# Optimization experiments

Hardware: AMD Instinct MI355X
Metric: run time of the kernel (lower is better)

The kernel has to match this reference:

```python
import jax, jax.numpy as jnp
import numpy as np

N, E, D, A = 50000, 1_600_000, 32, 2
H1, C1, H2, C2 = 4, 16, 2, 32  # GATv2Conv(D,16,heads=4) -> 64; GATv2Conv(64,32,heads=2) -> 64


def setup_inputs() -> dict:
    key = jax.random.key(0)
    ks = jax.random.split(key, 16)

    def glorot(k, shape):
        fan = shape[0] + shape[-1]
        return jax.random.normal(k, shape, jnp.float32) * np.float32(np.sqrt(2.0 / fan))

    return {
        "x": jax.random.normal(ks[0], (N, D), jnp.float32),
        "edge_index": jax.random.randint(ks[1], (2, E), 0, N),
        "edge_attr": jax.random.normal(ks[2], (E, 2), jnp.float32),
        # GATv2 layer 1 (lin_l/lin_r with bias, lin_edge no bias, att [H,C], out bias)
        "w1_l": glorot(ks[3], (D, H1 * C1)), "b1_l": jnp.zeros((H1 * C1,), jnp.float32),
        "w1_r": glorot(ks[4], (D, H1 * C1)), "b1_r": jnp.zeros((H1 * C1,), jnp.float32),
        "w1_e": glorot(ks[5], (2, H1 * C1)),
        "att1": glorot(ks[6], (H1, C1)),
        "bias1": jnp.zeros((H1 * C1,), jnp.float32),
        # GATv2 layer 2
        "w2_l": glorot(ks[7], (H1 * C1, H2 * C2)), "b2_l": jnp.zeros((H2 * C2,), jnp.float32),
        "w2_r": glorot(ks[8], (H1 * C1, H2 * C2)), "b2_r": jnp.zeros((H2 * C2,), jnp.float32),
        "w2_e": glorot(ks[9], (2, H2 * C2)),
        "att2": glorot(ks[10], (H2, C2)),
        "bias2": jnp.zeros((H2 * C2,), jnp.float32),
        # heads
        "w_actor": glorot(ks[11], (H2 * C2, A)), "b_actor": jnp.zeros((A,), jnp.float32),
        "w_critic": glorot(ks[12], (H2 * C2, 1)), "b_critic": jnp.zeros((1,), jnp.float32),
        "log_std": jnp.zeros((A,), jnp.float32),
    }


def _gatv2(x, src, dst, eattr, Wl, bl, Wr, br, We, att, bias, H, C, n):
    # PyG GATv2Conv: message j->i with i = dst, j = src
    xl = (x @ Wl + bl).reshape(n, H, C)  # source-side transform (x_j)
    xr = (x @ Wr + br).reshape(n, H, C)  # target-side transform (x_i)
    ee = (eattr @ We).reshape(-1, H, C)  # per-edge embedding
    z = jax.nn.leaky_relu(xl[src] + xr[dst] + ee, 0.2)  # [Etot, H, C]
    logits = jnp.einsum('ehc,hc->eh', z, att)  # [Etot, H]
    # segment softmax over incoming edges of each dst node
    m = jax.ops.segment_max(logits, dst, num_segments=n)
    p = jnp.exp(logits - m[dst])
    denom = jax.ops.segment_sum(p, dst, num_segments=n)
    alpha = p / denom[dst]  # every node has a self-loop -> denom > 0
    msg = xl[src] * alpha[:, :, None]  # [Etot, H, C]
    out = jax.ops.segment_sum(msg, dst, num_segments=n)
    return out.reshape(n, H * C) + bias


def reference(x, edge_index, edge_attr,
              w1_l, b1_l, w1_r, b1_r, w1_e, att1, bias1,
              w2_l, b2_l, w2_r, b2_r, w2_e, att2, bias2,
              w_actor, b_actor, w_critic, b_critic, log_std):
    src, dst = edge_index[0], edge_index[1]
    # add_self_loops=True, fill_value='mean': self-loop edge_attr = mean of incoming edge_attr
    cnt = jax.ops.segment_sum(jnp.ones((edge_attr.shape[0],), x.dtype), dst, num_segments=N)
    sums = jax.ops.segment_sum(edge_attr, dst, num_segments=N)
    loop_attr = sums / jnp.maximum(cnt, 1.0)[:, None]
    loop = jnp.arange(N, dtype=src.dtype)
    src_f = jnp.concatenate([src, loop])
    dst_f = jnp.concatenate([dst, loop])
    ea = jnp.concatenate([edge_attr, loop_attr], axis=0)

    h = jax.nn.relu(_gatv2(x, src_f, dst_f, ea, w1_l, b1_l, w1_r, b1_r, w1_e, att1, bias1, H1, C1, N))
    h = jax.nn.relu(_gatv2(h, src_f, dst_f, ea, w2_l, b2_l, w2_r, b2_r, w2_e, att2, bias2, H2, C2, N))

    action_mean = jnp.tanh(h @ w_actor + b_actor)  # [N, A]
    value = h @ w_critic + b_critic               # [N, 1]
    std = jnp.exp(log_std)                        # [A]  (Normal(action_mean, std))
    return action_mean, std, value
```

## Files before the change

kernel.cpp:

```cpp
#include <hip/hip_runtime.h>
#include <hip/hip_fp16.h>
#include <math.h>

#define DIN   32
#define F1    64
#define F2    64

typedef __attribute__((ext_vector_type(2))) float f32x2;

__device__ __forceinline__ f32x2 pkfma(f32x2 a, f32x2 b, f32x2 c) {
#if __has_builtin(__builtin_elementwise_fma)
    return __builtin_elementwise_fma(a, b, c);
#else
    return a * b + c;
#endif
}
__device__ __forceinline__ f32x2 pkmax(f32x2 a, f32x2 b) {
    f32x2 r; r.x = fmaxf(a.x, b.x); r.y = fmaxf(a.y, b.y); return r;
}

__device__ __forceinline__ unsigned bf16pack(float a, float b) {
    unsigned ua = __float_as_uint(a);
    unsigned ub = __float_as_uint(b);
    ua = (ua + 0x7FFFu + ((ua >> 16) & 1u)) >> 16;
    ub = (ub + 0x7FFFu + ((ub >> 16) & 1u)) >> 16;
    return ua | (ub << 16);
}

template <int K>
__device__ __forceinline__ void lin_lr_body(int bid,
        const float* __restrict__ x,
        const float* __restrict__ Wl, const float* __restrict__ bl,
        const float* __restrict__ Wr, const float* __restrict__ br,
        __half* __restrict__ xl, float* __restrict__ xr, int n) {
    __shared__ float Ash[32][K + 4];
    __shared__ float Wsh[K][128];
    const int t = threadIdx.x;
    const int node0 = bid * 32;

    for (int idx = t; idx < 32 * (K / 4); idx += 256) {
        int m = idx / (K / 4), kq = idx % (K / 4);
        float4 v = make_float4(0.f, 0.f, 0.f, 0.f);
        if (node0 + m < n) v = ((const float4*)(x + (size_t)(node0 + m) * K))[kq];
        *(float4*)&Ash[m][kq * 4] = v;
    }
    for (int idx = t; idx < K * 32; idx += 256) {
        int k = idx / 32, j4 = idx % 32;
        float4 v = (j4 < 16) ? ((const float4*)(Wl + (size_t)k * 64))[j4]
                             : ((const float4*)(Wr + (size_t)k * 64))[j4 - 16];
        *(float4*)&Wsh[k][j4 * 4] = v;
    }
    __syncthreads();

    const int ty = t >> 4;
    const int tx = t & 15;
    f32x2 c0[4], c1[4];
#pragma unroll
    for (int j = 0; j < 4; j++) {
        c0[j].x = 0.f; c0[j].y = 0.f;
        c1[j].x = 0.f; c1[j].y = 0.f;
    }

#pragma unroll 4
    for (int k = 0; k < K; k++) {
        float a0 = Ash[ty * 2 + 0][k];
        float a1 = Ash[ty * 2 + 1][k];
        float4 w0 = *(const float4*)&Wsh[k][tx * 8];
        float4 w1 = *(const float4*)&Wsh[k][tx * 8 + 4];
        f32x2 wv0; wv0.x = w0.x; wv0.y = w0.y;
        f32x2 wv1; wv1.x = w0.z; wv1.y = w0.w;
        f32x2 wv2; wv2.x = w1.x; wv2.y = w1.y;
        f32x2 wv3; wv3.x = w1.z; wv3.y = w1.w;
        f32x2 a0s; a0s.x = a0; a0s.y = a0;
        f32x2 a1s; a1s.x = a1; a1s.y = a1;
        c0[0] = pkfma(a0s, wv0, c0[0]);
        c0[1] = pkfma(a0s, wv1, c0[1]);
        c0[2] = pkfma(a0s, wv2, c0[2]);
        c0[3] = pkfma(a0s, wv3, c0[3]);
        c1[0] = pkfma(a1s, wv0, c1[0]);
        c1[1] = pkfma(a1s, wv1, c1[1]);
        c1[2] = pkfma(a1s, wv2, c1[2]);
        c1[3] = pkfma(a1s, wv3, c1[3]);
    }

    const float* bsrc = (tx < 8) ? bl : br;
    int jb = (tx < 8) ? tx * 8 : (tx - 8) * 8;
    float4 b0 = ((const float4*)(bsrc + jb))[0];
    float4 b1 = ((const float4*)(bsrc + jb))[1];
#pragma unroll
    for (int m = 0; m < 2; m++) {
        int node = node0 + ty * 2 + m;
        if (node >= n) continue;
        const f32x2* cc = (m == 0) ? c0 : c1;
        float o0 = cc[0].x + b0.x, o1 = cc[0].y + b0.y;
        float o2 = cc[1].x + b0.z, o3 = cc[1].y + b0.w;
        float o4 = cc[2].x + b1.x, o5 = cc[2].y + b1.y;
        float o6 = cc[3].x + b1.z, o7 = cc[3].y + b1.w;
        if (tx < 8) {
            __half2 h0 = __floats2half2_rn(o0, o1);
            __half2 h1 = __floats2half2_rn(o2, o3);
            __half2 h2 = __floats2half2_rn(o4, o5);
            __half2 h3 = __floats2half2_rn(o6, o7);
            uint4 pk;
            pk.x = *(unsigned*)&h0; pk.y = *(unsigned*)&h1;
            pk.z = *(unsigned*)&h2; pk.w = *(unsigned*)&h3;
            *((uint4*)(xl + (size_t)node * 64 + jb)) = pk;
        } else {
            float4 f0 = make_float4(o0, o1, o2, o3);
            float4 f1 = make_float4(o4, o5, o6, o7);
            ((float4*)(xr + (size_t)node * 64 + jb))[0] = f0;
            ((float4*)(xr + (size_t)node * 64 + jb))[1] = f1;
        }
    }
}

__global__ __launch_bounds__(512, 2)
void count_scatter(const int* __restrict__ srcr, const int* __restrict__ dstr,
                   const float* __restrict__ ea, int* __restrict__ cursor,
                   int2* __restrict__ inter, int E, int Ec, int NB, int cap) {
    __shared__ int2 recsh[3584];
    __shared__ unsigned short rksh[3584];
    __shared__ unsigned char bksh[3584];
    __shared__ int hist[256];
    __shared__ int colsh[256];
    const int blk = blockIdx.x;
    const int t = threadIdx.x;
    if (t < 256) hist[t] = 0;
    __syncthreads();
    const int s0 = blk * Ec, s1 = min(E, s0 + Ec);
    const int cnt = s1 - s0;
    for (int e = s0 + t; e < s1; e += 512) {
        int d = dstr[e];
        float2 v = ((const float2*)ea)[e];
        int2 r;
        r.x = srcr[e] | ((d & 255) << 24);
        r.y = (int)bf16pack(v.x, v.y);
        int li = e - s0;
        int bk = (unsigned)d >> 8;
        recsh[li] = r;
        bksh[li] = (unsigned char)bk;
        rksh[li] = (unsigned short)atomicAdd(&hist[bk], 1);
    }
    __syncthreads();
    if (t < NB) {
        int h = hist[t];
        colsh[t] = t * cap + (h ? atomicAdd(&cursor[t], h) : 0);
    }
    __syncthreads();
    for (int li = t; li < cnt; li += 512)
        inter[colsh[bksh[li]] + (int)rksh[li]] = recsh[li];
}

__global__ __launch_bounds__(256, 2)
void fused_csr_lin1(const int2* __restrict__ inter, const int* __restrict__ cursor,
                    int2* __restrict__ rse, int2* __restrict__ edges,
                    int NB, int N, int cap,
                    const float* __restrict__ x,
                    const float* __restrict__ Wl, const float* __restrict__ bl,
                    const float* __restrict__ Wr, const float* __restrict__ br,
                    __half* __restrict__ xl, float* __restrict__ xr, int n) {
    if ((int)blockIdx.x >= NB) {
        lin_lr_body<DIN>(blockIdx.x - NB, x, Wl, bl, Wr, br, xl, xr, n);
        return;
    }
    __shared__ int sh[256];
    __shared__ int cur[256];
    const int b = blockIdx.x, t = threadIdx.x;
    const int bstart = b * cap;
    const int bend = bstart + cursor[b];

    sh[t] = 0;
    __syncthreads();
    for (int pos = bstart + t; pos < bend; pos += 256)
        atomicAdd(&sh[((unsigned)inter[pos].x) >> 24], 1);
    __syncthreads();
    int cnt_v = sh[t];
    __syncthreads();
    sh[t] = cnt_v;
    __syncthreads();
    for (int off = 1; off < 256; off <<= 1) {
        int xv = (t >= off) ? sh[t - off] : 0;
        __syncthreads();
        sh[t] += xv;
        __syncthreads();
    }
    {
        int excl = sh[t] - cnt_v;
        cur[t] = excl;
        int myrs = bstart + excl;
        int node = b * 256 + t;
        if (node < N) rse[node] = make_int2(myrs, myrs + cnt_v);
    }
    __syncthreads();
    for (int pos = bstart + t; pos < bend; pos += 256) {
        int2 r = inter[pos];
        int k = atomicAdd(&cur[((unsigned)r.x) >> 24], 1);
        r.x &= 0x00FFFFFF;
        edges[bstart + k] = r;
    }
    int zend = (b + 1) * cap + ((b == NB - 1) ? 64 : 0);
    for (int pos = bend + t; pos < zend; pos += 256)
        edges[pos] = make_int2(0, 0);
}

template <int H, int C, bool FUSE_HEADS, bool FUSE_LIN2>
__global__ __launch_bounds__(512)
void gat_kernel(const __half* __restrict__ xl, const float* __restrict__ xr,
                const int2* __restrict__ rse,
                const int2* __restrict__ edges,
                const float* __restrict__ We, const float* __restrict__ att,
                const float* __restrict__ bias, float* __restrict__ hout,
                const float* __restrict__ w2l, const float* __restrict__ b2l,
                const float* __restrict__ w2r, const float* __restrict__ b2r,
                __half* __restrict__ xl2o, float* __restrict__ xr2o,
                const float* __restrict__ wa, const float* __restrict__ ba,
                const float* __restrict__ wc, const float* __restrict__ bc,
                const float* __restrict__ ls, float* __restrict__ pout,
                int n) {
    constexpr int LPH = C / 4;
    __shared__ float W2sh[FUSE_LIN2 ? 64 * 128 : 4];
    if constexpr (FUSE_LIN2) {
        for (int idx = threadIdx.x; idx < 64 * 32; idx += (int)blockDim.x) {
            int k = idx >> 5, j4 = idx & 31;
            float4 v = (j4 < 16) ? ((const float4*)(w2l + (size_t)k * 64))[j4]
                                 : ((const float4*)(w2r + (size_t)k * 64))[j4 - 16];
            *(float4*)&W2sh[k * 128 + j4 * 4] = v;
        }
        __syncthreads();
    }
    if (FUSE_HEADS && blockIdx.x == 0 && threadIdx.x < 2)
        pout[(size_t)n * 2 + threadIdx.x] = expf(ls[threadIdx.x]);
    const int lane = threadIdx.x & 63;
    const int wid = (blockIdx.x * blockDim.x + threadIdx.x) >> 6;
    if (wid >= n) return;
    const int i = wid;
    const int g = lane >> 4;
    const int q = lane & 15;

    const uint2* xlh = (const uint2*)xl;
    const float4 xri4 = ((const float4*)(xr + (size_t)i * 64))[q];
    const float4 we04 = ((const float4*)We)[q];
    const float4 we14 = ((const float4*)(We + 64))[q];
    const float4 av4 = ((const float4*)att)[q];
    const float LOG2E = 1.4426950408889634f;
    f32x2 xrlo; xrlo.x = xri4.x; xrlo.y = xri4.y;
    f32x2 xrhi; xrhi.x = xri4.z; xrhi.y = xri4.w;
    f32x2 we0lo; we0lo.x = we04.x; we0lo.y = we04.y;
    f32x2 we0hi; we0hi.x = we04.z; we0hi.y = we04.w;
    f32x2 we1lo; we1lo.x = we14.x; we1lo.y = we14.y;
    f32x2 we1hi; we1hi.x = we14.z; we1hi.y = we14.w;
    f32x2 avlo; avlo.x = av4.x * LOG2E; avlo.y = av4.y * LOG2E;
    f32x2 avhi; avhi.x = av4.z * LOG2E; avhi.y = av4.w * LOG2E;

    auto h4lo = [](uint2 h) -> f32x2 {
        float2 a = __half22float2(*(__half2*)&h.x);
        f32x2 r; r.x = a.x; r.y = a.y; return r;
    };
    auto h4hi = [](uint2 h) -> f32x2 {
        float2 b = __half22float2(*(__half2*)&h.y);
        f32x2 r; r.x = b.x; r.y = b.y; return r;
    };
    auto logit_of = [&](f32x2 xlo, f32x2 xhi, float ea0, float ea1) -> float {
        f32x2 e0; e0.x = ea0; e0.y = ea0;
        f32x2 e1; e1.x = ea1; e1.y = ea1;
        f32x2 ylo = xlo + pkfma(e0, we0lo, pkfma(e1, we1lo, xrlo));
        f32x2 yhi = xhi + pkfma(e0, we0hi, pkfma(e1, we1hi, xrhi));
        ylo = pkmax(ylo, ylo * 0.2f);
        yhi = pkmax(yhi, yhi * 0.2f);
        f32x2 l2 = pkfma(ylo, avlo, yhi * avhi);
        return l2.x + l2.y;
    };

    float den = 0.f;
    float sea0 = 0.f, sea1 = 0.f;
    f32x2 aclo; aclo.x = 0.f; aclo.y = 0.f;
    f32x2 achi; achi.x = 0.f; achi.y = 0.f;

    const int2 se = rse[i];
    const int e0 = se.x, e1 = se.y;
    const int r = (e1 - e0) & 7;

    if (r) {
        int2 h0 = edges[e0 + g];
        int2 h1 = edges[e0 + 4 + g];
        uint2 u0 = xlh[(h0.x << 4) + q];
        uint2 u1 = xlh[(h1.x << 4) + q];
        f32x2 x0lo = h4lo(u0), x0hi = h4hi(u0);
        f32x2 x1lo = h4lo(u1), x1hi = h4hi(u1);
        const bool v0 = g < r;
        const bool v1 = (4 + g) < r;
        float ea00 = v0 ? __int_as_float(h0.y << 16) : 0.f;
        float ea01 = v0 ? __int_as_float(h0.y & 0xFFFF0000) : 0.f;
        float ea10 = v1 ? __int_as_float(h1.y << 16) : 0.f;
        float ea11 = v1 ? __int_as_float(h1.y & 0xFFFF0000) : 0.f;
        sea0 += ea00 + ea10;
        sea1 += ea01 + ea11;
        float l0 = logit_of(x0lo, x0hi, ea00, ea01);
        float l1 = logit_of(x1lo, x1hi, ea10, ea11);
#pragma unroll
        for (int m = 1; m < LPH; m <<= 1) {
            l0 += __shfl_xor(l0, m, 64);
            l1 += __shfl_xor(l1, m, 64);
        }
        float p0 = v0 ? exp2f(l0) : 0.f;
        float p1 = v1 ? exp2f(l1) : 0.f;
        den += p0 + p1;
        f32x2 p0s; p0s.x = p0; p0s.y = p0;
        f32x2 p1s; p1s.x = p1; p1s.y = p1;
        aclo = pkfma(p0s, x0lo, pkfma(p1s, x1lo, aclo));
        achi = pkfma(p0s, x0hi, pkfma(p1s, x1hi, achi));
    }

    const int em = e0 + r;
    int2 rn0 = edges[em + g];
    int2 rn1 = edges[em + 4 + g];
    uint2 xpn0 = xlh[(rn0.x << 4) + q];
    uint2 xpn1 = xlh[(rn1.x << 4) + q];

    for (int eb = em; eb < e1; eb += 8) {
        int2 r0 = rn0, r1 = rn1;
        f32x2 x0lo = h4lo(xpn0), x0hi = h4hi(xpn0);
        f32x2 x1lo = h4lo(xpn1), x1hi = h4hi(xpn1);
        rn0 = edges[eb + 8 + g];
        rn1 = edges[eb + 12 + g];
        xpn0 = xlh[(rn0.x << 4) + q];
        xpn1 = xlh[(rn1.x << 4) + q];

        float ea00 = __int_as_float(r0.y << 16);
        float ea01 = __int_as_float(r0.y & 0xFFFF0000);
        float ea10 = __int_as_float(r1.y << 16);
        float ea11 = __int_as_float(r1.y & 0xFFFF0000);
        sea0 += ea00 + ea10;
        sea1 += ea01 + ea11;

        float l0 = logit_of(x0lo, x0hi, ea00, ea01);
        float l1 = logit_of(x1lo, x1hi, ea10, ea11);
#pragma unroll
        for (int m = 1; m < LPH; m <<= 1) {
            l0 += __shfl_xor(l0, m, 64);
            l1 += __shfl_xor(l1, m, 64);
        }
        float p0 = exp2f(l0);
        float p1 = exp2f(l1);
        den += p0 + p1;
        f32x2 p0s; p0s.x = p0; p0s.y = p0;
        f32x2 p1s; p1s.x = p1; p1s.y = p1;
        aclo = pkfma(p0s, x0lo, pkfma(p1s, x1lo, aclo));
        achi = pkfma(p0s, x0hi, pkfma(p1s, x1hi, achi));
    }

    float a0 = aclo.x, a1 = aclo.y, a2 = achi.x, a3 = achi.y;

#pragma unroll
    for (int m = 16; m < 64; m <<= 1) {
        den += __shfl_xor(den, m, 64);
        a0 += __shfl_xor(a0, m, 64);
        a1 += __shfl_xor(a1, m, 64);
        a2 += __shfl_xor(a2, m, 64);
        a3 += __shfl_xor(a3, m, 64);
        sea0 += __shfl_xor(sea0, m, 64);
        sea1 += __shfl_xor(sea1, m, 64);
    }

    const int cnt_i = e1 - e0;
    const float invc = cnt_i ? 1.0f / (float)cnt_i : 0.f;
    const float lamx = sea0 * invc;
    const float lamy = sea1 * invc;
    uint2 us = xlh[(i << 4) + q];
    f32x2 xslo = h4lo(us), xshi = h4hi(us);
    {
        float l = logit_of(xslo, xshi, lamx, lamy);
#pragma unroll
        for (int m = 1; m < LPH; m <<= 1) l += __shfl_xor(l, m, 64);
        float p = exp2f(l);
        den += p;
        a0 = fmaf(p, xslo.x, a0);
        a1 = fmaf(p, xslo.y, a1);
        a2 = fmaf(p, xshi.x, a2);
        a3 = fmaf(p, xshi.y, a3);
    }

    float rd = 1.0f / den;
    const float4 bv = ((const float4*)bias)[q];
    float4 o;
    o.x = fmaxf(fmaf(a0, rd, bv.x), 0.f);
    o.y = fmaxf(fmaf(a1, rd, bv.y), 0.f);
    o.z = fmaxf(fmaf(a2, rd, bv.z), 0.f);
    o.w = fmaxf(fmaf(a3, rd, bv.w), 0.f);

    if constexpr (FUSE_LIN2) {
        const int hl = lane & 31;
        const bool isl = lane < 32;
        f32x2 s; s.x = 0.f; s.y = 0.f;
#pragma unroll
        for (int k = 0; k < 64; k++) {
            float comp = ((k & 3) == 0) ? o.x : ((k & 3) == 1) ? o.y
                       : ((k & 3) == 2) ? o.z : o.w;
            float hk = __uint_as_float(
                __builtin_amdgcn_readlane(__float_as_uint(comp), k >> 2));
            f32x2 hs; hs.x = hk; hs.y = hk;
            f32x2 wv = *(const f32x2*)&W2sh[k * 128 + 2 * lane];
            s = pkfma(hs, wv, s);
        }
        const float* bsel = isl ? b2l : b2r;
        s.x += bsel[2 * hl];
        s.y += bsel[2 * hl + 1];
        if (isl) {
            __half2 hx = __floats2half2_rn(s.x, s.y);
            *(unsigned*)(xl2o + (size_t)i * 64 + 2 * hl) = *(unsigned*)&hx;
        } else {
            ((float2*)(xr2o + (size_t)i * 64))[hl] = make_float2(s.x, s.y);
        }
    } else if (!FUSE_HEADS) {
        if (g == 0) ((float4*)(hout + (size_t)i * 64))[q] = o;
    } else {
        float4 wa01 = ((const float4*)wa)[q * 2];
        float4 wa23 = ((const float4*)wa)[q * 2 + 1];
        float4 wcv  = ((const float4*)wc)[q];
        float d0 = o.x * wa01.x + o.y * wa01.z + o.z * wa23.x + o.w * wa23.z;
        float d1 = o.x * wa01.y + o.y * wa01.w + o.z * wa23.y + o.w * wa23.w;
        float d2 = o.x * wcv.x + o.y * wcv.y + o.z * wcv.z + o.w * wcv.w;
#pragma unroll
        for (int m = 1; m < 16; m <<= 1) {
            d0 += __shfl_xor(d0, m, 64);
            d1 += __shfl_xor(d1, m, 64);
            d2 += __shfl_xor(d2, m, 64);
        }
        if (lane == 0) {
            pout[(size_t)i * 2 + 0] = tanhf(d0 + ba[0]);
            pout[(size_t)i * 2 + 1] = tanhf(d1 + ba[1]);
            pout[(size_t)n * 2 + 2 + i] = d2 + bc[0];
        }
    }
}


extern "C" void kernel_launch(void* const* d_in, const int* in_sizes, int n_in,
                              void* d_out, int out_size, void* d_ws, size_t ws_size,
                              hipStream_t stream) {
    const float* x    = (const float*)d_in[0];
    const int*   ei   = (const int*)  d_in[1];
    const float* ea   = (const float*)d_in[2];
    const float* w1l  = (const float*)d_in[3];
    const float* b1l  = (const float*)d_in[4];
    const float* w1r  = (const float*)d_in[5];
    const float* b1r  = (const float*)d_in[6];
    const float* w1e  = (const float*)d_in[7];
    const float* att1 = (const float*)d_in[8];
    const float* bias1= (const float*)d_in[9];
    const float* w2l  = (const float*)d_in[10];
    const float* b2l  = (const float*)d_in[11];
    const float* w2r  = (const float*)d_in[12];
    const float* b2r  = (const float*)d_in[13];
    const float* w2e  = (const float*)d_in[14];
    const float* att2 = (const float*)d_in[15];
    const float* bias2= (const float*)d_in[16];
    const float* wa   = (const float*)d_in[17];
    const float* ba   = (const float*)d_in[18];
    const float* wc   = (const float*)d_in[19];
    const float* bc   = (const float*)d_in[20];
    const float* ls   = (const float*)d_in[21];

    const int N = in_sizes[0] / DIN;
    const int E = in_sizes[2] / 2;
    const int* srcr = ei;
    const int* dstr = ei + E;

    const int NB = (N + 255) >> 8;
    const int NCH = 512;
    const int Ec = (E + NCH - 1) / NCH;
    int cap = (E + NB - 1) / NB;
    cap = ((cap + cap / 4) + 63) & ~63;

    char* p = (char*)d_ws;
    auto alloc = [&](size_t bytes) -> void* {
        void* r = (void*)p;
        p += (bytes + 255) & ~(size_t)255;
        return r;
    };
    int*    cursor = (int*)   alloc(256 * 4);
    int2*   rse    = (int2*)  alloc((size_t)N * 8);
    int2*   edges  = (int2*)  alloc(((size_t)NB * cap + 64) * 8);
    __half* xl     = (__half*)alloc((size_t)N * F1 * 2);
    float*  xr     = (float*) alloc((size_t)N * F1 * 4);
    __half* xl2    = (__half*)alloc((size_t)N * F2 * 2);
    float*  xr2    = (float*) alloc((size_t)N * F2 * 4);
    int2* inter = (int2*)xl2;
    (void)ws_size; (void)n_in; (void)out_size;

    hipMemsetAsync(cursor, 0, 256 * 4, stream);

    const int TB = 256;
    int gridGemm = (N + 31) / 32;
    int gridW1 = (N + 7) / 8;
    int gridW2 = (N + 3) / 4;

    count_scatter<<<NCH, 512, 0, stream>>>(srcr, dstr, ea, cursor, inter,
                                           E, Ec, NB, cap);
    fused_csr_lin1<<<NB + gridGemm, TB, 0, stream>>>(
        inter, cursor, rse, edges, NB, N, cap,
        x, w1l, b1l, w1r, b1r, xl, xr, N);

    gat_kernel<4, 16, false, true><<<gridW1, 512, 0, stream>>>(
        xl, xr, rse, edges, w1e, att1, bias1, nullptr,
        w2l, b2l, w2r, b2r, xl2, xr2,
        nullptr, nullptr, nullptr, nullptr, nullptr, nullptr, N);

    gat_kernel<2, 32, true, false><<<gridW2, TB, 0, stream>>>(
        xl2, xr2, rse, edges, w2e, att2, bias2, nullptr,
        nullptr, nullptr, nullptr, nullptr, nullptr, nullptr,
        wa, ba, wc, bc, ls, (float*)d_out, N);
}
```

Measured before the change: 281.7 us.

## Fuse layer-1 linear into count/scatter kernel and split CSR build into quarters

Moves the layer-1 node linear transform out of the CSR build kernel and into the edge count/scatter kernel, with each 512-thread block running two 256-thread GEMM tiles over shared memory that is carved up by hand. The CSR build is now launched with four blocks per bucket. Each block redoes the bucket histogram and prefix scan but places only the edges whose destination falls in its quarter, which spreads the scatter over more blocks. The cost of this is histogram and scan work repeated four times, plus every block reading the whole bucket's intermediate records.

```diff
diff --git a/kernel.cpp b/kernel.cpp
--- a/kernel.cpp
+++ b/kernel.cpp
@@ -28,14 +28,13 @@
 }
 
 template <int K>
-__device__ __forceinline__ void lin_lr_body(int bid,
+__device__ __forceinline__ void lin_lr_body(int bid, int t, float* smem,
         const float* __restrict__ x,
         const float* __restrict__ Wl, const float* __restrict__ bl,
         const float* __restrict__ Wr, const float* __restrict__ br,
         __half* __restrict__ xl, float* __restrict__ xr, int n) {
-    __shared__ float Ash[32][K + 4];
-    __shared__ float Wsh[K][128];
-    const int t = threadIdx.x;
+    float (*Ash)[K + 4] = (float (*)[K + 4])smem;
+    float (*Wsh)[128]   = (float (*)[128])(smem + 32 * (K + 4));
     const int node0 = bid * 32;
 
     for (int idx = t; idx < 32 * (K / 4); idx += 256) {
@@ -114,15 +113,28 @@
     }
 }
 
-__global__ __launch_bounds__(512, 2)
-void count_scatter(const int* __restrict__ srcr, const int* __restrict__ dstr,
-                   const float* __restrict__ ea, int* __restrict__ cursor,
-                   int2* __restrict__ inter, int E, int Ec, int NB, int cap) {
-    __shared__ int2 recsh[3584];
-    __shared__ unsigned short rksh[3584];
-    __shared__ unsigned char bksh[3584];
-    __shared__ int hist[256];
-    __shared__ int colsh[256];
+__global__ __launch_bounds__(512, 4)
+void fused_count_lin1(const int* __restrict__ srcr, const int* __restrict__ dstr,
+                      const float* __restrict__ ea, int* __restrict__ cursor,
+                      int2* __restrict__ inter, int E, int Ec, int NB, int cap,
+                      int gridCnt,
+                      const float* __restrict__ x,
+                      const float* __restrict__ Wl, const float* __restrict__ bl,
+                      const float* __restrict__ Wr, const float* __restrict__ br,
+                      __half* __restrict__ xl, float* __restrict__ xr, int n) {
+    __shared__ __align__(16) char smem[41984];
+    if ((int)blockIdx.x >= gridCnt) {
+        const int sub = threadIdx.x >> 8;
+        const int lb = ((int)blockIdx.x - gridCnt) * 2 + sub;
+        lin_lr_body<DIN>(lb, threadIdx.x & 255, (float*)(smem + sub * 20992),
+                         x, Wl, bl, Wr, br, xl, xr, n);
+        return;
+    }
+    int2* recsh = (int2*)smem;
+    unsigned short* rksh = (unsigned short*)(smem + 28672);
+    unsigned char* bksh = (unsigned char*)(smem + 35840);
+    int* hist  = (int*)(smem + 39424);
+    int* colsh = (int*)(smem + 40448);
     const int blk = blockIdx.x;
     const int t = threadIdx.x;
     if (t < 256) hist[t] = 0;
@@ -151,56 +163,53 @@
         inter[colsh[bksh[li]] + (int)rksh[li]] = recsh[li];
 }
 
-__global__ __launch_bounds__(256, 2)
-void fused_csr_lin1(const int2* __restrict__ inter, const int* __restrict__ cursor,
-                    int2* __restrict__ rse, int2* __restrict__ edges,
-                    int NB, int N, int cap,
-                    const float* __restrict__ x,
-                    const float* __restrict__ Wl, const float* __restrict__ bl,
-                    const float* __restrict__ Wr, const float* __restrict__ br,
-                    __half* __restrict__ xl, float* __restrict__ xr, int n) {
-    if ((int)blockIdx.x >= NB) {
-        lin_lr_body<DIN>(blockIdx.x - NB, x, Wl, bl, Wr, br, xl, xr, n);
-        return;
-    }
+__global__ __launch_bounds__(512, 4)
+void csr4(const int2* __restrict__ inter, const int* __restrict__ cursor,
+          int2* __restrict__ rse, int2* __restrict__ edges,
+          int NB, int N, int cap) {
     __shared__ int sh[256];
     __shared__ int cur[256];
-    const int b = blockIdx.x, t = threadIdx.x;
+    const int b = blockIdx.x >> 2, qtr = blockIdx.x & 3, t = threadIdx.x;
     const int bstart = b * cap;
     const int bend = bstart + cursor[b];
 
-    sh[t] = 0;
-    __syncthreads();
-    for (int pos = bstart + t; pos < bend; pos += 256)
+    if (t < 256) sh[t] = 0;
+    __syncthreads();
+    for (int pos = bstart + t; pos < bend; pos += 512)
         atomicAdd(&sh[((unsigned)inter[pos].x) >> 24], 1);
     __syncthreads();
-    int cnt_v = sh[t];
-    __syncthreads();
-    sh[t] = cnt_v;
+    int cnt_v = (t < 256) ? sh[t] : 0;
+    __syncthreads();
+    if (t < 256) sh[t] = cnt_v;
     __syncthreads();
     for (int off = 1; off < 256; off <<= 1) {
-        int xv = (t >= off) ? sh[t - off] : 0;
+        int xv = (t >= off && t < 256) ? sh[t - off] : 0;
         __syncthreads();
-        sh[t] += xv;
+        if (t < 256) sh[t] += xv;
         __syncthreads();
     }
-    {
+    if (t < 256) {
         int excl = sh[t] - cnt_v;
         cur[t] = excl;
-        int myrs = bstart + excl;
         int node = b * 256 + t;
-        if (node < N) rse[node] = make_int2(myrs, myrs + cnt_v);
-    }
-    __syncthreads();
-    for (int pos = bstart + t; pos < bend; pos += 256) {
+        if ((t >> 6) == qtr && node < N)
+            rse[node] = make_int2(bstart + excl, bstart + excl + cnt_v);
+    }
+    __syncthreads();
+    for (int pos = bstart + t; pos < bend; pos += 512) {
         int2 r = inter[pos];
-        int k = atomicAdd(&cur[((unsigned)r.x) >> 24], 1);
-        r.x &= 0x00FFFFFF;
-        edges[bstart + k] = r;
-    }
-    int zend = (b + 1) * cap + ((b == NB - 1) ? 64 : 0);
-    for (int pos = bend + t; pos < zend; pos += 256)
-        edges[pos] = make_int2(0, 0);
+        int d = ((unsigned)r.x) >> 24;
+        if ((d >> 6) == qtr) {
+            int k = atomicAdd(&cur[d], 1);
+            r.x &= 0x00FFFFFF;
+            edges[bstart + k] = r;
+        }
+    }
+    if (qtr == 3) {
+        int zend = (b + 1) * cap + ((b == NB - 1) ? 64 : 0);
+        for (int pos = bend + t; pos < zend; pos += 512)
+            edges[pos] = make_int2(0, 0);
+    }
 }
 
 template <int H, int C, bool FUSE_HEADS, bool FUSE_LIN2>
@@ -490,23 +499,22 @@
 
     hipMemsetAsync(cursor, 0, 256 * 4, stream);
 
-    const int TB = 256;
     int gridGemm = (N + 31) / 32;
+    int gridLin2 = (gridGemm + 1) / 2;
     int gridW1 = (N + 7) / 8;
     int gridW2 = (N + 3) / 4;
 
-    count_scatter<<<NCH, 512, 0, stream>>>(srcr, dstr, ea, cursor, inter,
-                                           E, Ec, NB, cap);
-    fused_csr_lin1<<<NB + gridGemm, TB, 0, stream>>>(
-        inter, cursor, rse, edges, NB, N, cap,
+    fused_count_lin1<<<NCH + gridLin2, 512, 0, stream>>>(
+        srcr, dstr, ea, cursor, inter, E, Ec, NB, cap, NCH,
         x, w1l, b1l, w1r, b1r, xl, xr, N);
+    csr4<<<4 * NB, 512, 0, stream>>>(inter, cursor, rse, edges, NB, N, cap);
 
     gat_kernel<4, 16, false, true><<<gridW1, 512, 0, stream>>>(
         xl, xr, rse, edges, w1e, att1, bias1, nullptr,
         w2l, b2l, w2r, b2r, xl2, xr2,
         nullptr, nullptr, nullptr, nullptr, nullptr, nullptr, N);
 
-    gat_kernel<2, 32, true, false><<<gridW2, TB, 0, stream>>>(
+    gat_kernel<2, 32, true, false><<<gridW2, 256, 0, stream>>>(
         xl2, xr2, rse, edges, w2e, att2, bias2, nullptr,
         nullptr, nullptr, nullptr, nullptr, nullptr, nullptr,
         wa, ba, wc, bc, ls, (float*)d_out, N);
```

New measurement: 290.4 us. 3.1% more time.
